# Optimization experiments

Hardware: AMD Instinct MI355X
Metric: run time of the kernel (lower is better)

## Reference

```python
import jax, jax.numpy as jnp
import numpy as np

NUM_QUBITS = 12
NUM_LAYERS = 2
STATE_DIM = 2 ** NUM_QUBITS
BATCH = 4096
TWO_PI = 2 * 3.1416  # matches the original initializer constant


def _u3(theta, phi, lam):
    """Single-qubit U3 gate, 2x2 complex64 (matches TF layer exactly)."""
    c = jnp.cos(theta / 2)
    s = jnp.sin(theta / 2)
    z = jnp.zeros_like(phi)
    e_phi = jnp.exp(jax.lax.complex(z, phi))
    e_lam = jnp.exp(jax.lax.complex(z, lam))
    e_pl = jnp.exp(jax.lax.complex(z, phi + lam))
    cc = jax.lax.complex(c, jnp.zeros_like(c))
    sc = jax.lax.complex(s, jnp.zeros_like(s))
    row1 = jnp.stack([cc, -e_lam * sc])
    row2 = jnp.stack([e_phi * sc, e_pl * cc])
    return jnp.stack([row1, row2])  # [2, 2] complex64


def _full_gate(theta_vec, phi_vec, lam_vec):
    """Kronecker product of per-qubit gates -> [2^n, 2^n] complex64."""
    full = _u3(theta_vec[0], phi_vec[0], lam_vec[0])
    for q in range(1, theta_vec.shape[0]):
        full = jnp.kron(full, _u3(theta_vec[q], phi_vec[q], lam_vec[q]))
    return full


def setup_inputs() -> dict:
    key = jax.random.key(0)
    k1, k2, k3, k4 = jax.random.split(key, 4)
    inputs = jax.random.normal(k1, (BATCH, STATE_DIM), dtype=jnp.float32)
    thetas = jax.random.uniform(k2, (NUM_LAYERS, NUM_QUBITS), minval=0.0, maxval=TWO_PI, dtype=jnp.float32)
    phis = jax.random.uniform(k3, (NUM_LAYERS, NUM_QUBITS), minval=0.0, maxval=TWO_PI, dtype=jnp.float32)
    lams = jax.random.uniform(k4, (NUM_LAYERS, NUM_QUBITS), minval=0.0, maxval=TWO_PI, dtype=jnp.float32)
    return {"inputs": inputs, "thetas": thetas, "phis": phis, "lams": lams}


def reference(inputs, thetas, phis, lams):
    # normalize real inputs as complex state, per-sample L2 norm
    state = jax.lax.complex(inputs, jnp.zeros_like(inputs))  # [B, D] complex64
    norm = jnp.linalg.norm(state, axis=1, keepdims=True)      # real, [B, 1]
    state = state / norm
    for l in range(thetas.shape[0]):
        U = _full_gate(thetas[l], phis[l], lams[l])  # [D, D]
        # matvec(U, x) per sample == state @ U^T, batched GEMM replaces tf.map_fn
        state = state @ U.T
    return jnp.real(state * jnp.conj(state))  # probabilities, [B, D] float32
```

## Files before the change

kernel.cpp:

```cpp
#include <hip/hip_runtime.h>

#define NQ   12
#define DIM  4096
#define NL   2
#define BATCH 4096

__global__ void build_gates(const float* __restrict__ th,
                            const float* __restrict__ ph,
                            const float* __restrict__ lm,
                            float* __restrict__ gates) {
    int q = threadIdx.x;
    if (q >= NQ) return;
    float g00r = 1.f, g00i = 0.f, g01r = 0.f, g01i = 0.f;
    float g10r = 0.f, g10i = 0.f, g11r = 1.f, g11i = 0.f;
    for (int l = 0; l < NL; ++l) {
        float th2 = 0.5f * th[l * NQ + q];
        float p   = ph[l * NQ + q];
        float la  = lm[l * NQ + q];
        float c = cosf(th2), s = sinf(th2);
        float u00r = c,                u00i = 0.f;
        float u01r = -cosf(la) * s,    u01i = -sinf(la) * s;
        float u10r = cosf(p) * s,      u10i = sinf(p) * s;
        float u11r = cosf(p + la) * c, u11i = sinf(p + la) * c;
        float n00r = u00r*g00r - u00i*g00i + u01r*g10r - u01i*g10i;
        float n00i = u00r*g00i + u00i*g00r + u01r*g10i + u01i*g10r;
        float n01r = u00r*g01r - u00i*g01i + u01r*g11r - u01i*g11i;
        float n01i = u00r*g01i + u00i*g01r + u01r*g11i + u01i*g11r;
        float n10r = u10r*g00r - u10i*g00i + u11r*g10r - u11i*g10i;
        float n10i = u10r*g00i + u10i*g00r + u11r*g10i + u11i*g10r;
        float n11r = u10r*g01r - u10i*g01i + u11r*g11r - u11i*g11i;
        float n11i = u10r*g01i + u10i*g01r + u11r*g11i + u11i*g11r;
        g00r = n00r; g00i = n00i; g01r = n01r; g01i = n01i;
        g10r = n10r; g10i = n10i; g11r = n11r; g11i = n11i;
    }
    int k = (NQ - 1) - q;
    float* o = gates + k * 8;
    o[0] = g00r; o[1] = g00i; o[2] = g01r; o[3] = g01i;
    o[4] = g10r; o[5] = g10i; o[6] = g11r; o[7] = g11i;
}

struct Gate { float r00, i00, r01, i01, r10, i10, r11, i11; };

__device__ __forceinline__ Gate load_gate(const float* __restrict__ g, int k) {
    const float* p = g + k * 8;
    Gate q;
    q.r00 = p[0]; q.i00 = p[1]; q.r01 = p[2]; q.i01 = p[3];
    q.r10 = p[4]; q.i10 = p[5]; q.r11 = p[6]; q.i11 = p[7];
    return q;
}

__device__ __forceinline__ int lds_off(int idx) { return idx + (idx >> 4); }

__device__ __forceinline__ void apply_gate(float vr[16], float vi[16],
                                           int r0, int r1, const Gate& g) {
    float x0r = vr[r0], x0i = vi[r0], x1r = vr[r1], x1i = vi[r1];
    vr[r0] = g.r00 * x0r - g.i00 * x0i + g.r01 * x1r - g.i01 * x1i;
    vi[r0] = g.r00 * x0i + g.i00 * x0r + g.r01 * x1i + g.i01 * x1r;
    vr[r1] = g.r10 * x0r - g.i10 * x0i + g.r11 * x1r - g.i11 * x1i;
    vi[r1] = g.r10 * x0i + g.i10 * x0r + g.r11 * x1i + g.i11 * x1r;
}

__device__ __forceinline__ void apply_on_rbit(float vr[16], float vi[16],
                                              int rb, const Gate& g) {
    const int m = 1 << rb;
    #pragma unroll
    for (int h = 0; h < 8; ++h) {
        int low = h & (m - 1);
        int r   = ((h & ~(m - 1)) << 1) | low;
        apply_gate(vr, vi, r, r | m, g);
    }
}

__global__ __launch_bounds__(256, 4)
void qc_sim(const float* __restrict__ in, const float* __restrict__ gates,
            float* __restrict__ out) {
    __shared__ float sre[DIM + DIM / 16];
    __shared__ float simg[DIM + DIM / 16];
    __shared__ float red[4];

    const int t = threadIdx.x;
    const int b = blockIdx.x;

    float vr[16], vi[16];
    float ss = 0.f;

    const float4* __restrict__ x4 =
        reinterpret_cast<const float4*>(in + (size_t)b * DIM);
    #pragma unroll
    for (int j = 0; j < 4; ++j) {
        float4 v = x4[j * 256 + t];
        int r = j * 4;
        vr[r] = v.x; vr[r + 1] = v.y; vr[r + 2] = v.z; vr[r + 3] = v.w;
        ss += v.x * v.x + v.y * v.y + v.z * v.z + v.w * v.w;
    }
    #pragma unroll
    for (int off = 32; off > 0; off >>= 1)
        ss += __shfl_down(ss, off, 64);
    if ((t & 63) == 0) red[t >> 6] = ss;

    {
        Gate g0 = load_gate(gates, 0);
        #pragma unroll
        for (int r = 0; r < 16; r += 2) {
            float x0 = vr[r], x1 = vr[r + 1];
            vr[r]     = g0.r00 * x0 + g0.r01 * x1;
            vi[r]     = g0.i00 * x0 + g0.i01 * x1;
            vr[r + 1] = g0.r10 * x0 + g0.r11 * x1;
            vi[r + 1] = g0.i10 * x0 + g0.i11 * x1;
        }
        Gate g1 = load_gate(gates, 1);
        apply_on_rbit(vr, vi, 1, g1);
        Gate ga = load_gate(gates, 10);
        apply_on_rbit(vr, vi, 2, ga);
        Gate gb = load_gate(gates, 11);
        apply_on_rbit(vr, vi, 3, gb);
    }
    #pragma unroll
    for (int r = 0; r < 16; ++r) {
        int idx = ((r >> 2) << 10) + t * 4 + (r & 3);
        int o = lds_off(idx);
        sre[o] = vr[r]; simg[o] = vi[r];
    }
    __syncthreads();

    #pragma unroll
    for (int r = 0; r < 16; ++r) {
        int idx = ((t >> 2) << 6) + (r << 2) + (t & 3);
        int o = lds_off(idx);
        vr[r] = sre[o]; vi[r] = simg[o];
    }
    {
        Gate g2 = load_gate(gates, 2);
        apply_on_rbit(vr, vi, 0, g2);
        Gate g3 = load_gate(gates, 3);
        apply_on_rbit(vr, vi, 1, g3);
        Gate g4 = load_gate(gates, 4);
        apply_on_rbit(vr, vi, 2, g4);
        Gate g5 = load_gate(gates, 5);
        apply_on_rbit(vr, vi, 3, g5);
    }
    #pragma unroll
    for (int r = 0; r < 16; ++r) {
        int idx = ((t >> 2) << 6) + (r << 2) + (t & 3);
        int o = lds_off(idx);
        sre[o] = vr[r]; simg[o] = vi[r];
    }
    __syncthreads();

    #pragma unroll
    for (int r = 0; r < 16; ++r) {
        int idx = ((t >> 6) << 10) + (r << 6) + (t & 63);
        int o = lds_off(idx);
        vr[r] = sre[o]; vi[r] = simg[o];
    }
    {
        Gate g6 = load_gate(gates, 6);
        apply_on_rbit(vr, vi, 0, g6);
        Gate g7 = load_gate(gates, 7);
        apply_on_rbit(vr, vi, 1, g7);
        Gate g8 = load_gate(gates, 8);
        apply_on_rbit(vr, vi, 2, g8);
        Gate g9 = load_gate(gates, 9);
        apply_on_rbit(vr, vi, 3, g9);
    }

    float tot = red[0] + red[1] + red[2] + red[3];
    float inv = 1.0f / tot;
    float* __restrict__ o = out + (size_t)b * DIM;
    #pragma unroll
    for (int r = 0; r < 16; ++r) {
        int idx = ((t >> 6) << 10) + (r << 6) + (t & 63);
        o[idx] = (vr[r] * vr[r] + vi[r] * vi[r]) * inv;
    }
}

extern "C" void kernel_launch(void* const* d_in, const int* in_sizes, int n_in,
                              void* d_out, int out_size, void* d_ws, size_t ws_size,
                              hipStream_t stream) {
    (void)in_sizes; (void)n_in; (void)out_size; (void)ws_size;
    const float* inputs = (const float*)d_in[0];
    const float* thetas = (const float*)d_in[1];
    const float* phis   = (const float*)d_in[2];
    const float* lams   = (const float*)d_in[3];
    float* gates = (float*)d_ws;
    float* out   = (float*)d_out;

    hipLaunchKernelGGL(build_gates, dim3(1), dim3(64), 0, stream,
                       thetas, phis, lams, gates);
    hipLaunchKernelGGL(qc_sim, dim3(BATCH), dim3(256), 0, stream,
                       inputs, gates, out);
}
```

Before: 143.0 us.

## Fuse gate construction into simulator and use packed float2 complex arithmetic

Removes the separate gate-building kernel launch by having each block compute the 12 fused single-qubit gates into shared memory. Complex amplitudes are stored as float2 vectors so gate application can use packed FP32 FMAs, and LDS now stores interleaved real/imag pairs. An extra barrier is added before reusing the LDS buffer. The trade-off is redundant trig work per block and a different LDS access width.

```diff
diff --git a/kernel.cpp b/kernel.cpp
--- a/kernel.cpp
+++ b/kernel.cpp
@@ -5,164 +5,152 @@
 #define NL   2
 #define BATCH 4096
 
-__global__ void build_gates(const float* __restrict__ th,
-                            const float* __restrict__ ph,
-                            const float* __restrict__ lm,
-                            float* __restrict__ gates) {
-    int q = threadIdx.x;
-    if (q >= NQ) return;
-    float g00r = 1.f, g00i = 0.f, g01r = 0.f, g01i = 0.f;
-    float g10r = 0.f, g10i = 0.f, g11r = 1.f, g11i = 0.f;
-    for (int l = 0; l < NL; ++l) {
-        float th2 = 0.5f * th[l * NQ + q];
-        float p   = ph[l * NQ + q];
-        float la  = lm[l * NQ + q];
-        float c = cosf(th2), s = sinf(th2);
-        float u00r = c,                u00i = 0.f;
-        float u01r = -cosf(la) * s,    u01i = -sinf(la) * s;
-        float u10r = cosf(p) * s,      u10i = sinf(p) * s;
-        float u11r = cosf(p + la) * c, u11i = sinf(p + la) * c;
-        float n00r = u00r*g00r - u00i*g00i + u01r*g10r - u01i*g10i;
-        float n00i = u00r*g00i + u00i*g00r + u01r*g10i + u01i*g10r;
-        float n01r = u00r*g01r - u00i*g01i + u01r*g11r - u01i*g11i;
-        float n01i = u00r*g01i + u00i*g01r + u01r*g11i + u01i*g11r;
-        float n10r = u10r*g00r - u10i*g00i + u11r*g10r - u11i*g10i;
-        float n10i = u10r*g00i + u10i*g00r + u11r*g10i + u11i*g10r;
-        float n11r = u10r*g01r - u10i*g01i + u11r*g11r - u11i*g11i;
-        float n11i = u10r*g01i + u10i*g01r + u11r*g11i + u11i*g11r;
-        g00r = n00r; g00i = n00i; g01r = n01r; g01i = n01i;
-        g10r = n10r; g10i = n10i; g11r = n11r; g11i = n11i;
-    }
-    int k = (NQ - 1) - q;
-    float* o = gates + k * 8;
-    o[0] = g00r; o[1] = g00i; o[2] = g01r; o[3] = g01i;
-    o[4] = g10r; o[5] = g10i; o[6] = g11r; o[7] = g11i;
+typedef float v2f __attribute__((ext_vector_type(2)));
+
+
+struct PGate { v2f a00, b00, a01, b01, a10, b10, a11, b11; };
+
+__device__ __forceinline__ PGate make_pg(const float* __restrict__ g) {
+    PGate p;
+    float r00 = g[0], i00 = g[1], r01 = g[2], i01 = g[3];
+    float r10 = g[4], i10 = g[5], r11 = g[6], i11 = g[7];
+    p.a00 = (v2f){ r00, i00 };  p.b00 = (v2f){ -i00, r00 };
+    p.a01 = (v2f){ r01, i01 };  p.b01 = (v2f){ -i01, r01 };
+    p.a10 = (v2f){ r10, i10 };  p.b10 = (v2f){ -i10, r10 };
+    p.a11 = (v2f){ r11, i11 };  p.b11 = (v2f){ -i11, r11 };
+    return p;
 }
 
-struct Gate { float r00, i00, r01, i01, r10, i10, r11, i11; };
-
-__device__ __forceinline__ Gate load_gate(const float* __restrict__ g, int k) {
-    const float* p = g + k * 8;
-    Gate q;
-    q.r00 = p[0]; q.i00 = p[1]; q.r01 = p[2]; q.i01 = p[3];
-    q.r10 = p[4]; q.i10 = p[5]; q.r11 = p[6]; q.i11 = p[7];
-    return q;
+__device__ __forceinline__ void papply(v2f v[16], int r0, int r1, const PGate& g) {
+    v2f x0 = v[r0], x1 = v[r1];
+    v2f x0r = (v2f){ x0.x, x0.x }, x0i = (v2f){ x0.y, x0.y };
+    v2f x1r = (v2f){ x1.x, x1.x }, x1i = (v2f){ x1.y, x1.y };
+    v[r0] = g.a00 * x0r + g.b00 * x0i + g.a01 * x1r + g.b01 * x1i;
+    v[r1] = g.a10 * x0r + g.b10 * x0i + g.a11 * x1r + g.b11 * x1i;
 }
 
-__device__ __forceinline__ int lds_off(int idx) { return idx + (idx >> 4); }
-
-__device__ __forceinline__ void apply_gate(float vr[16], float vi[16],
-                                           int r0, int r1, const Gate& g) {
-    float x0r = vr[r0], x0i = vi[r0], x1r = vr[r1], x1i = vi[r1];
-    vr[r0] = g.r00 * x0r - g.i00 * x0i + g.r01 * x1r - g.i01 * x1i;
-    vi[r0] = g.r00 * x0i + g.i00 * x0r + g.r01 * x1i + g.i01 * x1r;
-    vr[r1] = g.r10 * x0r - g.i10 * x0i + g.r11 * x1r - g.i11 * x1i;
-    vi[r1] = g.r10 * x0i + g.i10 * x0r + g.r11 * x1i + g.i11 * x1r;
-}
-
-__device__ __forceinline__ void apply_on_rbit(float vr[16], float vi[16],
-                                              int rb, const Gate& g) {
+__device__ __forceinline__ void papply_rbit(v2f v[16], int rb, const PGate& g) {
     const int m = 1 << rb;
     #pragma unroll
     for (int h = 0; h < 8; ++h) {
         int low = h & (m - 1);
         int r   = ((h & ~(m - 1)) << 1) | low;
-        apply_gate(vr, vi, r, r | m, g);
+        papply(v, r, r | m, g);
     }
 }
 
+__device__ __forceinline__ int lds_off(int idx) { return idx + (idx >> 4); }
+
 __global__ __launch_bounds__(256, 4)
-void qc_sim(const float* __restrict__ in, const float* __restrict__ gates,
+void qc_sim(const float* __restrict__ in,
+            const float* __restrict__ th,
+            const float* __restrict__ ph,
+            const float* __restrict__ lm,
             float* __restrict__ out) {
-    __shared__ float sre[DIM + DIM / 16];
-    __shared__ float simg[DIM + DIM / 16];
+    __shared__ v2f   st[DIM + DIM / 16];
+    __shared__ float sg[NQ][8];
     __shared__ float red[4];
 
     const int t = threadIdx.x;
     const int b = blockIdx.x;
 
-    float vr[16], vi[16];
+    v2f v[16];
     float ss = 0.f;
 
     const float4* __restrict__ x4 =
         reinterpret_cast<const float4*>(in + (size_t)b * DIM);
     #pragma unroll
     for (int j = 0; j < 4; ++j) {
-        float4 v = x4[j * 256 + t];
+        float4 w = x4[j * 256 + t];
         int r = j * 4;
-        vr[r] = v.x; vr[r + 1] = v.y; vr[r + 2] = v.z; vr[r + 3] = v.w;
-        ss += v.x * v.x + v.y * v.y + v.z * v.z + v.w * v.w;
+        v[r]     = (v2f){ w.x, 0.f };
+        v[r + 1] = (v2f){ w.y, 0.f };
+        v[r + 2] = (v2f){ w.z, 0.f };
+        v[r + 3] = (v2f){ w.w, 0.f };
+        ss += w.x * w.x + w.y * w.y + w.z * w.z + w.w * w.w;
     }
     #pragma unroll
     for (int off = 32; off > 0; off >>= 1)
         ss += __shfl_down(ss, off, 64);
     if ((t & 63) == 0) red[t >> 6] = ss;
 
+    if (t < NQ) {
+        int q = t;
+        float g00r = 1.f, g00i = 0.f, g01r = 0.f, g01i = 0.f;
+        float g10r = 0.f, g10i = 0.f, g11r = 1.f, g11i = 0.f;
+        #pragma unroll
+        for (int l = 0; l < NL; ++l) {
+            float th2 = 0.5f * th[l * NQ + q];
+            float p   = ph[l * NQ + q];
+            float la  = lm[l * NQ + q];
+            float c = cosf(th2), s = sinf(th2);
+            float u00r = c,                u00i = 0.f;
+            float u01r = -cosf(la) * s,    u01i = -sinf(la) * s;
+            float u10r = cosf(p) * s,      u10i = sinf(p) * s;
+            float u11r = cosf(p + la) * c, u11i = sinf(p + la) * c;
+            float n00r = u00r*g00r - u00i*g00i + u01r*g10r - u01i*g10i;
+            float n00i = u00r*g00i + u00i*g00r + u01r*g10i + u01i*g10r;
+            float n01r = u00r*g01r - u00i*g01i + u01r*g11r - u01i*g11i;
+            float n01i = u00r*g01i + u00i*g01r + u01r*g11i + u01i*g11r;
+            float n10r = u10r*g00r - u10i*g00i + u11r*g10r - u11i*g10i;
+            float n10i = u10r*g00i + u10i*g00r + u11r*g10i + u11i*g10r;
+            float n11r = u10r*g01r - u10i*g01i + u11r*g11r - u11i*g11i;
+            float n11i = u10r*g01i + u10i*g01r + u11r*g11i + u11i*g11r;
+            g00r = n00r; g00i = n00i; g01r = n01r; g01i = n01i;
+            g10r = n10r; g10i = n10i; g11r = n11r; g11i = n11i;
+        }
+        int k = (NQ - 1) - q;
+        sg[k][0] = g00r; sg[k][1] = g00i; sg[k][2] = g01r; sg[k][3] = g01i;
+        sg[k][4] = g10r; sg[k][5] = g10i; sg[k][6] = g11r; sg[k][7] = g11i;
+    }
+    __syncthreads();
+
     {
-        Gate g0 = load_gate(gates, 0);
+        PGate g0 = make_pg(sg[0]);
         #pragma unroll
         for (int r = 0; r < 16; r += 2) {
-            float x0 = vr[r], x1 = vr[r + 1];
-            vr[r]     = g0.r00 * x0 + g0.r01 * x1;
-            vi[r]     = g0.i00 * x0 + g0.i01 * x1;
-            vr[r + 1] = g0.r10 * x0 + g0.r11 * x1;
-            vi[r + 1] = g0.i10 * x0 + g0.i11 * x1;
+            v2f x0r = (v2f){ v[r].x,     v[r].x     };
+            v2f x1r = (v2f){ v[r + 1].x, v[r + 1].x };
+            v[r]     = g0.a00 * x0r + g0.a01 * x1r;
+            v[r + 1] = g0.a10 * x0r + g0.a11 * x1r;
         }
-        Gate g1 = load_gate(gates, 1);
-        apply_on_rbit(vr, vi, 1, g1);
-        Gate ga = load_gate(gates, 10);
-        apply_on_rbit(vr, vi, 2, ga);
-        Gate gb = load_gate(gates, 11);
-        apply_on_rbit(vr, vi, 3, gb);
+        { PGate g = make_pg(sg[1]);  papply_rbit(v, 1, g); }
+        { PGate g = make_pg(sg[10]); papply_rbit(v, 2, g); }
+        { PGate g = make_pg(sg[11]); papply_rbit(v, 3, g); }
     }
     #pragma unroll
     for (int r = 0; r < 16; ++r) {
         int idx = ((r >> 2) << 10) + t * 4 + (r & 3);
-        int o = lds_off(idx);
-        sre[o] = vr[r]; simg[o] = vi[r];
+        st[lds_off(idx)] = v[r];
     }
     __syncthreads();
 
     #pragma unroll
     for (int r = 0; r < 16; ++r) {
         int idx = ((t >> 2) << 6) + (r << 2) + (t & 3);
-        int o = lds_off(idx);
-        vr[r] = sre[o]; vi[r] = simg[o];
+        v[r] = st[lds_off(idx)];
     }
-    {
-        Gate g2 = load_gate(gates, 2);
-        apply_on_rbit(vr, vi, 0, g2);
-        Gate g3 = load_gate(gates, 3);
-        apply_on_rbit(vr, vi, 1, g3);
-        Gate g4 = load_gate(gates, 4);
-        apply_on_rbit(vr, vi, 2, g4);
-        Gate g5 = load_gate(gates, 5);
-        apply_on_rbit(vr, vi, 3, g5);
-    }
+    { PGate g = make_pg(sg[2]); papply_rbit(v, 0, g); }
+    { PGate g = make_pg(sg[3]); papply_rbit(v, 1, g); }
+    { PGate g = make_pg(sg[4]); papply_rbit(v, 2, g); }
+    { PGate g = make_pg(sg[5]); papply_rbit(v, 3, g); }
+    __syncthreads();
     #pragma unroll
     for (int r = 0; r < 16; ++r) {
         int idx = ((t >> 2) << 6) + (r << 2) + (t & 3);
-        int o = lds_off(idx);
-        sre[o] = vr[r]; simg[o] = vi[r];
+        st[lds_off(idx)] = v[r];
     }
     __syncthreads();
 
     #pragma unroll
     for (int r = 0; r < 16; ++r) {
         int idx = ((t >> 6) << 10) + (r << 6) + (t & 63);
-        int o = lds_off(idx);
-        vr[r] = sre[o]; vi[r] = simg[o];
+        v[r] = st[lds_off(idx)];
     }
-    {
-        Gate g6 = load_gate(gates, 6);
-        apply_on_rbit(vr, vi, 0, g6);
-        Gate g7 = load_gate(gates, 7);
-        apply_on_rbit(vr, vi, 1, g7);
-        Gate g8 = load_gate(gates, 8);
-        apply_on_rbit(vr, vi, 2, g8);
-        Gate g9 = load_gate(gates, 9);
-        apply_on_rbit(vr, vi, 3, g9);
-    }
+    { PGate g = make_pg(sg[6]); papply_rbit(v, 0, g); }
+    { PGate g = make_pg(sg[7]); papply_rbit(v, 1, g); }
+    { PGate g = make_pg(sg[8]); papply_rbit(v, 2, g); }
+    { PGate g = make_pg(sg[9]); papply_rbit(v, 3, g); }
 
     float tot = red[0] + red[1] + red[2] + red[3];
     float inv = 1.0f / tot;
@@ -170,23 +158,21 @@
     #pragma unroll
     for (int r = 0; r < 16; ++r) {
         int idx = ((t >> 6) << 10) + (r << 6) + (t & 63);
-        o[idx] = (vr[r] * vr[r] + vi[r] * vi[r]) * inv;
+        v2f p2 = v[r] * v[r];
+        o[idx] = (p2.x + p2.y) * inv;
     }
 }
 
 extern "C" void kernel_launch(void* const* d_in, const int* in_sizes, int n_in,
                               void* d_out, int out_size, void* d_ws, size_t ws_size,
                               hipStream_t stream) {
-    (void)in_sizes; (void)n_in; (void)out_size; (void)ws_size;
+    (void)in_sizes; (void)n_in; (void)out_size; (void)d_ws; (void)ws_size;
     const float* inputs = (const float*)d_in[0];
     const float* thetas = (const float*)d_in[1];
     const float* phis   = (const float*)d_in[2];
     const float* lams   = (const float*)d_in[3];
-    float* gates = (float*)d_ws;
-    float* out   = (float*)d_out;
+    float* out = (float*)d_out;
 
-    hipLaunchKernelGGL(build_gates, dim3(1), dim3(64), 0, stream,
-                       thetas, phis, lams, gates);
     hipLaunchKernelGGL(qc_sim, dim3(BATCH), dim3(256), 0, stream,
-                       inputs, gates, out);
+                       inputs, thetas, phis, lams, out);
 }
```

After: 137.4 us. -3.9%, faster.
